# Optimization experiments

Measured on AMD Instinct MI355X. Metric: run time of the kernel, lower is better.

The kernel has to match this reference:

```python
import jax, jax.numpy as jnp
import numpy as np

IN_F = 256
OUT_F = 256
ALPHA = 0.2  # LeakyReLU negative slope


def _xavier(key, shape, gain=1.414):
    fan_in, fan_out = shape[0], shape[1]
    limit = gain * np.sqrt(6.0 / (fan_in + fan_out))
    return jax.random.uniform(key, shape, jnp.float32, -limit, limit)


def setup_inputs() -> dict:
    key = jax.random.key(0)
    k1, k2, k3, k4, k5, k6 = jax.random.split(key, 6)
    B, N = 8, 2048
    h = jax.random.normal(k1, (B, N, IN_F), jnp.float32)
    adj = jax.random.randint(k2, (B, N, N), 0, 2, jnp.int32)
    lrgt1 = jax.random.normal(k3, (B, N, OUT_F), jnp.float32)
    W1 = _xavier(k4, (IN_F, IN_F))
    W2 = _xavier(k5, (OUT_F, OUT_F))
    a = _xavier(k6, (2 * IN_F, 1))
    return {"h": h, "adj": adj, "lrgt1": lrgt1, "W1": W1, "W2": W2, "a": a}


def reference(h, adj, lrgt1, W1, W2, a):
    # Wh: [B,N,in], wlrgt: [B,N,out]
    Wh = jnp.matmul(h, W1)
    wlrgt = jnp.matmul(lrgt1, W2)
    # additive attention scores: e[b,i,j] = leaky_relu(Wh_i @ a1 + Wh_j @ a2)
    a1 = a[:IN_F, 0]   # [in]
    a2 = a[IN_F:, 0]   # [in]
    Wh1 = jnp.einsum('bnc,c->bn', Wh, a1)  # [B,N]
    Wh2 = jnp.einsum('bnc,c->bn', Wh, a2)  # [B,N]
    e = jax.nn.leaky_relu(Wh1[:, :, None] + Wh2[:, None, :], ALPHA)  # [B,N,N]
    neg = jnp.float32(-9e15)
    masked = jnp.where(adj > 0, e, neg)
    attention = jax.nn.softmax(masked, axis=2)
    # dropout p=0.0 / eval mode -> identity
    h_prime = jnp.matmul(attention, Wh)      # [B,N,in]
    gt_prime = jnp.matmul(attention, wlrgt)  # [B,N,out]
    return (jax.nn.elu(h_prime), jax.nn.elu(gt_prime))
```

## Files before the change

kernel.cpp:

```cpp
#include <hip/hip_runtime.h>
#include <hip/hip_bf16.h>

#define IN_F 256
#define NN   2048
#define BB   8

typedef unsigned short u16;
typedef __attribute__((ext_vector_type(8))) short short8x;
typedef __attribute__((ext_vector_type(4))) float float4x;

__device__ __forceinline__ u16 f2b(float f) {
    union { float f; unsigned int u; } x; x.f = f;
    unsigned int r = x.u + 0x7FFFu + ((x.u >> 16) & 1u);
    return (u16)(r >> 16);
}

__device__ __forceinline__ void transp_body(const float* __restrict__ src,
                                            u16* __restrict__ dst,
                                            int R, int C, int tid,
                                            float (*tile)[33])
{
    const int per = (R / 32) * (C / 32);
    const int b  = tid / per;
    const int tt = tid % per;
    const int jt = tt / (C / 32);
    const int ct = tt % (C / 32);
    src += (long)b * R * C;
    dst += (long)b * R * C;

    const int tx = threadIdx.x & 31, ty = threadIdx.x >> 5;
#pragma unroll
    for (int i = 0; i < 4; ++i)
        tile[ty + i * 8][tx] = src[(long)(jt * 32 + ty + i * 8) * C + ct * 32 + tx];
    __syncthreads();
#pragma unroll
    for (int i = 0; i < 4; ++i)
        dst[(long)(ct * 32 + ty + i * 8) * R + jt * 32 + tx] = f2b(tile[tx][ty + i * 8]);
}

__global__ __launch_bounds__(256) void prep(const float* __restrict__ h,
                                            const float* __restrict__ g,
                                            const float* __restrict__ W1,
                                            const float* __restrict__ W2,
                                            const float* __restrict__ a,
                                            u16* __restrict__ HbfT,
                                            u16* __restrict__ GbfT,
                                            u16* __restrict__ W1T,
                                            u16* __restrict__ W2T,
                                            float* __restrict__ v1,
                                            float* __restrict__ v2)
{
    __shared__ float tile[32][33];
    __shared__ float s1[IN_F], s2[IN_F];
    const int bid = blockIdx.x;

    if (bid < 4096) {
        transp_body(h, HbfT, NN, IN_F, bid, tile);
    } else if (bid < 8192) {
        transp_body(g, GbfT, NN, IN_F, bid - 4096, tile);
    } else if (bid < 8256) {
        transp_body(W1, W1T, IN_F, IN_F, bid - 8192, tile);
    } else if (bid < 8320) {
        transp_body(W2, W2T, IN_F, IN_F, bid - 8256, tile);
    } else {
        const int t = threadIdx.x;
        s1[t] = a[t];
        s2[t] = a[IN_F + t];
        __syncthreads();
        float acc1 = 0.f, acc2 = 0.f;
        for (int c = 0; c < IN_F; ++c) {
            float w = W1[t * IN_F + c];
            acc1 += w * s1[c];
            acc2 += w * s2[c];
        }
        v1[t] = acc1;
        v2[t] = acc2;
    }
}

__global__ __launch_bounds__(256) void rowdots(const float* __restrict__ h,
                                               const float* __restrict__ v1,
                                               const float* __restrict__ v2,
                                               float* __restrict__ Wh1,
                                               float* __restrict__ Wh2)
{
    const int wave = threadIdx.x >> 6;
    const int lane = threadIdx.x & 63;
    const long row = (long)blockIdx.x * 4 + wave;
    const int c0 = lane * 4;

    float4 v  = *(const float4*)(h + row * IN_F + c0);
    float4 a1 = *(const float4*)(v1 + c0);
    float4 a2 = *(const float4*)(v2 + c0);

    float s1 = v.x * a1.x + v.y * a1.y + v.z * a1.z + v.w * a1.w;
    float s2 = v.x * a2.x + v.y * a2.y + v.z * a2.z + v.w * a2.w;
#pragma unroll
    for (int off = 32; off; off >>= 1) {
        s1 += __shfl_xor(s1, off, 64);
        s2 += __shfl_xor(s2, off, 64);
    }
    if (lane == 0) { Wh1[row] = s1; Wh2[row] = s2; }
}

#define KSTEP(ksv, BC, BN_, AC, AN_, do_a, jnxt)                              \
    {                                                                         \
        if (do_a) {                                                           \
            _Pragma("unroll") for (int rt = 0; rt < 4; ++rt)                  \
                AN_[rt] = *(const short8x*)&ab[(((ksv) + 1) * 4 + rt) * 512 + lane * 8]; \
        }                                                                     \
        _Pragma("unroll") for (int ct = 0; ct < 4; ++ct)                      \
            BN_[ct] = *(const short8x*)(Bp + ct * 16 * NN + (jnxt));          \
        _Pragma("unroll") for (int rt = 0; rt < 4; ++rt)                      \
            _Pragma("unroll") for (int ct = 0; ct < 4; ++ct)                  \
                acc[rt][ct] = __builtin_amdgcn_mfma_f32_16x16x32_bf16(AC[rt], BC[ct], acc[rt][ct], 0, 0, 0); \
    }

#define CHUNKD2(KCH, ADJ, W4)                                                 \
    {                                                                         \
        const int j0 = (KCH) * 128;                                           \
        union { short8x v; u16 e[8]; } pk0, pk1;                              \
        _Pragma("unroll") for (int u = 0; u < 4; ++u) {                       \
            const float wf[4] = {W4[u].x, W4[u].y, W4[u].z, W4[u].w};         \
            const int   av[4] = {ADJ[u].x, ADJ[u].y, ADJ[u].z, ADJ[u].w};     \
            _Pragma("unroll") for (int c = 0; c < 4; ++c) {                   \
                float x = wh1rr + wf[c];                                      \
                float e = fmaxf(x, 0.2f * x);                                 \
                float p = __expf(e - mv);                                     \
                p = (av[c] > 0) ? p : 0.0f;                                   \
                lloc += p;                                                    \
                u16 fv = f2b(p);                                              \
                if (u < 2) pk0.e[u * 4 + c] = fv;                             \
                else       pk1.e[(u - 2) * 4 + c] = fv;                       \
            }                                                                 \
        }                                                                     \
        u16* ab = &Afrag[(KCH) & 1][0];                                       \
        *(short8x*)&ab[wbase0]       = pk0.v;                                 \
        *(short8x*)&ab[wbase0 + 128] = pk1.v;                                 \
        asm volatile("s_waitcnt lgkmcnt(0)\n\ts_barrier" ::: "memory");       \
        _Pragma("unroll") for (int rt = 0; rt < 4; ++rt)                      \
            A0[rt] = *(const short8x*)&ab[rt * 512 + lane * 8];               \
        KSTEP(0, B0, B1, A0, A1, 1, j0 + 1 * 32 + bq8)                        \
        KSTEP(1, B1, B0, A1, A0, 1, j0 + 2 * 32 + bq8)                        \
        KSTEP(2, B0, B1, A0, A1, 1, j0 + 3 * 32 + bq8)                        \
        KSTEP(3, B1, B0, A1, A0, 0, (((KCH) < 15) ? (j0 + 128) : j0) + bq8)   \
        if ((KCH) < 14) {                                                     \
            __builtin_amdgcn_sched_barrier(0);                                \
            const int jp = ((KCH) + 2) * 128 + sg * 16;                       \
            _Pragma("unroll") for (int u = 0; u < 4; ++u)                     \
                W4[u]  = *(const float4*)(wh2b + jp + u * 4);                 \
            _Pragma("unroll") for (int u = 0; u < 4; ++u)                     \
                ADJ[u] = *(const int4*)(adj + adjR + jp + u * 4);             \
        }                                                                     \
    }

__global__ __launch_bounds__(512, 2) void attn_mfma(
    const int* __restrict__ adj,
    const u16* __restrict__ HbfT, const u16* __restrict__ GbfT,
    const float* __restrict__ Wh1, const float* __restrict__ Wh2,
    u16* __restrict__ PH, u16* __restrict__ PG)
{
    const int t = threadIdx.x;
    const int wave = t >> 6, lane = t & 63;
    const int bswz = ((blockIdx.x & 7) << 5) | (blockIdx.x >> 3);
    const int b = bswz >> 5;
    const long gi0 = (long)bswz * 64;

    __shared__ __align__(16) u16 Afrag[2][8192];
    __shared__ float sred[512];
    __shared__ float ssc[65];

    const int rr = t >> 3, sg = t & 7;
    const long adjR = (gi0 + rr) * (long)NN;
    const float* wh2b = Wh2 + (long)b * NN;
    const float wh1rr = Wh1[gi0 + rr];

    {
        float4 w = *(const float4*)(wh2b + t * 4);
        sred[t] = fmaxf(fmaxf(w.x, w.y), fmaxf(w.z, w.w));
    }
    __syncthreads();
    if (t < 64) {
        float v = sred[t * 8];
#pragma unroll
        for (int k = 1; k < 8; ++k) v = fmaxf(v, sred[t * 8 + k]);
#pragma unroll
        for (int off = 32; off; off >>= 1) v = fmaxf(v, __shfl_xor(v, off, 64));
        if (t == 0) ssc[64] = v;
    }
    __syncthreads();
    const float mm = wh1rr + ssc[64];
    const float mv = (mm >= 0.f) ? mm : 0.2f * mm;

    const int wbase0 = ((sg >> 1) * 4 + (rr >> 4)) * 512
                     + ((rr & 15) + 16 * (2 * (sg & 1))) * 8;

    float4x acc[4][4];
#pragma unroll
    for (int rt = 0; rt < 4; ++rt)
#pragma unroll
        for (int ct = 0; ct < 4; ++ct) acc[rt][ct] = (float4x)0.0f;

    const int bn = lane & 15, bq = lane >> 4, bq8 = bq * 8;
    const long hbase = (long)b * IN_F * NN;
    const u16* Bp = ((wave < 4) ? HbfT : GbfT) + hbase
                  + (long)((wave & 3) * 64 + bn) * NN;

    float lloc = 0.f;

    short8x A0[4], A1[4], B0[4], B1[4];
    int4   adjA[4], adjB[4];
    float4 w4A[4], w4B[4];

#pragma unroll
    for (int u = 0; u < 4; ++u) {
        w4A[u]  = *(const float4*)(wh2b + sg * 16 + u * 4);
        adjA[u] = *(const int4*)(adj + adjR + sg * 16 + u * 4);
    }
#pragma unroll
    for (int u = 0; u < 4; ++u) {
        w4B[u]  = *(const float4*)(wh2b + 128 + sg * 16 + u * 4);
        adjB[u] = *(const int4*)(adj + adjR + 128 + sg * 16 + u * 4);
    }
#pragma unroll
    for (int ct = 0; ct < 4; ++ct)
        B0[ct] = *(const short8x*)(Bp + ct * 16 * NN + bq8);

    for (int kp = 0; kp < 8; ++kp) {
        CHUNKD2(kp * 2,     adjA, w4A)
        CHUNKD2(kp * 2 + 1, adjB, w4B)
    }

    sred[t] = lloc;
    __syncthreads();
    if (t < 64) {
        float v = sred[t * 8];
#pragma unroll
        for (int k = 1; k < 8; ++k) v += sred[t * 8 + k];
        ssc[t] = 1.0f / v;
    }
    __syncthreads();

    u16* dst = (wave < 4) ? PH : PG;
    const int colb = (wave & 3) * 64;
#pragma unroll
    for (int rt = 0; rt < 4; ++rt)
#pragma unroll
        for (int ct = 0; ct < 4; ++ct) {
            const int c = colb + ct * 16 + bn;
#pragma unroll
            for (int reg = 0; reg < 4; ++reg) {
                const int rl = rt * 16 + bq * 4 + reg;
                const float il = ssc[rl];
                const long row = gi0 + rl;
                dst[row * IN_F + c] = f2b(acc[rt][ct][reg] * il);
            }
        }
}

__global__ __launch_bounds__(256) void epi2(const u16* __restrict__ PH,
                                            const u16* __restrict__ PG,
                                            const u16* __restrict__ W1T,
                                            const u16* __restrict__ W2T,
                                            float* __restrict__ out)
{
    int bid = blockIdx.x;
    const u16* X;
    const u16* WT;
    float* o;
    if (bid < 512) { X = PH; WT = W1T; o = out; }
    else           { X = PG; WT = W2T; o = out + (long)BB * NN * IN_F; bid -= 512; }

    const int t = threadIdx.x;
    const int wave = t >> 6, lane = t & 63;
    const long i0 = (long)bid * 32;

    __shared__ __align__(16) u16 Afrag[8 * 2 * 64 * 8];

    const int m = t >> 3, ks0 = t & 7, rt0 = m >> 4, lm = m & 15;
    const u16* xp = X + (i0 + m) * IN_F + ks0 * 32;
#pragma unroll
    for (int q = 0; q < 4; ++q) {
        short8x v = *(const short8x*)(xp + q * 8);
        *(short8x*)&Afrag[((ks0 * 2 + rt0) * 64 + lm + q * 16) * 8] = v;
    }
    __syncthreads();

    float4x acc[2][4];
#pragma unroll
    for (int rt = 0; rt < 2; ++rt)
#pragma unroll
        for (int ct = 0; ct < 4; ++ct) acc[rt][ct] = (float4x)0.0f;

    const int bn = lane & 15, bq = lane >> 4;
#pragma unroll
    for (int ks = 0; ks < 8; ++ks) {
        short8x A0 = *(const short8x*)&Afrag[((ks * 2 + 0) * 64 + lane) * 8];
        short8x A1 = *(const short8x*)&Afrag[((ks * 2 + 1) * 64 + lane) * 8];
#pragma unroll
        for (int ct = 0; ct < 4; ++ct) {
            const int n = wave * 64 + ct * 16 + bn;
            short8x Bw = *(const short8x*)(WT + n * IN_F + ks * 32 + bq * 8);
            acc[0][ct] = __builtin_amdgcn_mfma_f32_16x16x32_bf16(A0, Bw, acc[0][ct], 0, 0, 0);
            acc[1][ct] = __builtin_amdgcn_mfma_f32_16x16x32_bf16(A1, Bw, acc[1][ct], 0, 0, 0);
        }
    }

#pragma unroll
    for (int rt = 0; rt < 2; ++rt)
#pragma unroll
        for (int ct = 0; ct < 4; ++ct) {
            const int n = wave * 64 + ct * 16 + bn;
#pragma unroll
            for (int reg = 0; reg < 4; ++reg) {
                const long row = i0 + rt * 16 + bq * 4 + reg;
                float v = acc[rt][ct][reg];
                v = (v > 0.f) ? v : (__expf(v) - 1.f);
                o[row * IN_F + n] = v;
            }
        }
}

extern "C" void kernel_launch(void* const* d_in, const int* in_sizes, int n_in,
                              void* d_out, int out_size, void* d_ws, size_t ws_size,
                              hipStream_t stream)
{
    int ih = -1, ig = -1, iadj = -1, iw1 = -1, iw2 = -1, ia = -1;
    for (int i = 0; i < n_in; ++i) {
        int s = in_sizes[i];
        if      (s == BB * NN * NN)   { if (iadj < 0) iadj = i; }
        else if (s == BB * NN * IN_F) { if (ih < 0) ih = i; else if (ig < 0) ig = i; }
        else if (s == IN_F * IN_F)    { if (iw1 < 0) iw1 = i; else if (iw2 < 0) iw2 = i; }
        else if (s == 2 * IN_F)       { if (ia < 0) ia = i; }
    }
    if (ih < 0 || ig < 0 || iadj < 0 || iw1 < 0 || iw2 < 0 || ia < 0) {
        ih = 0; iadj = 1; ig = 2; iw1 = 3; iw2 = 4; ia = 5;
    }
    const float* h     = (const float*)d_in[ih];
    const int*   adj   = (const int*)  d_in[iadj];
    const float* lrgt1 = (const float*)d_in[ig];
    const float* W1    = (const float*)d_in[iw1];
    const float* W2    = (const float*)d_in[iw2];
    const float* a     = (const float*)d_in[ia];
    float* out = (float*)d_out;

    float* ws   = (float*)d_ws;
    float* v1   = ws;
    float* v2   = v1 + IN_F;
    float* Wh1  = v2 + IN_F;
    float* Wh2  = Wh1 + BB * NN;
    u16* W1T  = (u16*)(Wh2 + BB * NN);
    u16* W2T  = W1T + IN_F * IN_F;
    u16* HbfT = W2T + IN_F * IN_F;
    u16* GbfT = HbfT + (long)BB * IN_F * NN;
    u16* PH   = GbfT + (long)BB * IN_F * NN;
    u16* PG   = PH + (long)BB * NN * IN_F;

    const int nrows = BB * NN;

    prep     <<<8321,        256, 0, stream>>>(h, lrgt1, W1, W2, a,
                                               HbfT, GbfT, W1T, W2T, v1, v2);
    rowdots  <<<nrows / 4,   256, 0, stream>>>(h, v1, v2, Wh1, Wh2);
    attn_mfma<<<nrows / 64,  512, 0, stream>>>(adj, HbfT, GbfT, Wh1, Wh2, PH, PG);
    epi2     <<<2 * nrows / 32, 256, 0, stream>>>(PH, PG, W1T, W2T, out);
}
```

Before: 313.6 us.

## Pack adjacency into bitmask, stage Wh2 in LDS, vectorize transpose

Adds a pre-pass kernel that ballots the int32 adjacency matrix into 64-bit masks stored in the output buffer as scratch. The attention kernel then reads one 32-bit mask word per chunk instead of 16 int4 loads, which removes register-held prefetch buffers and the heavy streaming of the int32 matrix inside the MFMA loop. Wh2 is staged once into shared memory rather than reloaded from global per chunk. The transpose in prep now uses float4 loads and ushort4 stores. The adjacency is still read once in full, but with simple coalesced nontemporal loads. Using d_out as scratch assumes the epilogue fully overwrites it afterwards.

New measurement: 344.3 us. 1.1x slower.

```diff
diff --git a/kernel.cpp b/kernel.cpp
--- a/kernel.cpp
+++ b/kernel.cpp
@@ -6,6 +6,7 @@
 #define BB   8
 
 typedef unsigned short u16;
+typedef unsigned long long u64;
 typedef __attribute__((ext_vector_type(8))) short short8x;
 typedef __attribute__((ext_vector_type(4))) float float4x;
 
@@ -15,10 +16,24 @@
     return (u16)(r >> 16);
 }
 
-__device__ __forceinline__ void transp_body(const float* __restrict__ src,
-                                            u16* __restrict__ dst,
-                                            int R, int C, int tid,
-                                            float (*tile)[33])
+__global__ __launch_bounds__(256) void adjpack(const int* __restrict__ adj,
+                                               u64* __restrict__ mask)
+{
+    const int wid  = (blockIdx.x * 256 + threadIdx.x) >> 6;
+    const int lane = threadIdx.x & 63;
+#pragma unroll 4
+    for (int it = 0; it < 64; ++it) {
+        const long s = (long)it * 8192 + wid;
+        const int v = __builtin_nontemporal_load(adj + s * 64 + lane);
+        const u64 m = __ballot(v > 0);
+        if (lane == 0) mask[s] = m;
+    }
+}
+
+__device__ __forceinline__ void transp_body4(const float* __restrict__ src,
+                                             u16* __restrict__ dst,
+                                             int R, int C, int tid,
+                                             float (*tile)[33])
 {
     const int per = (R / 32) * (C / 32);
     const int b  = tid / per;
@@ -28,14 +43,21 @@
     src += (long)b * R * C;
     dst += (long)b * R * C;
 
-    const int tx = threadIdx.x & 31, ty = threadIdx.x >> 5;
-#pragma unroll
-    for (int i = 0; i < 4; ++i)
-        tile[ty + i * 8][tx] = src[(long)(jt * 32 + ty + i * 8) * C + ct * 32 + tx];
-    __syncthreads();
-#pragma unroll
-    for (int i = 0; i < 4; ++i)
-        dst[(long)(ct * 32 + ty + i * 8) * R + jt * 32 + tx] = f2b(tile[tx][ty + i * 8]);
+    const int t = threadIdx.x;
+    const int lr = t >> 3, lc = (t & 7) * 4;
+    float4 v = *(const float4*)(src + (long)(jt * 32 + lr) * C + ct * 32 + lc);
+    tile[lr][lc + 0] = v.x;
+    tile[lr][lc + 1] = v.y;
+    tile[lr][lc + 2] = v.z;
+    tile[lr][lc + 3] = v.w;
+    __syncthreads();
+    const int c = t >> 3, r4 = (t & 7) * 4;
+    ushort4 o;
+    o.x = f2b(tile[r4 + 0][c]);
+    o.y = f2b(tile[r4 + 1][c]);
+    o.z = f2b(tile[r4 + 2][c]);
+    o.w = f2b(tile[r4 + 3][c]);
+    *(ushort4*)(dst + (long)(ct * 32 + c) * R + jt * 32 + r4) = o;
 }
 
 __global__ __launch_bounds__(256) void prep(const float* __restrict__ h,
@@ -55,13 +77,13 @@
     const int bid = blockIdx.x;
 
     if (bid < 4096) {
-        transp_body(h, HbfT, NN, IN_F, bid, tile);
+        transp_body4(h, HbfT, NN, IN_F, bid, tile);
     } else if (bid < 8192) {
-        transp_body(g, GbfT, NN, IN_F, bid - 4096, tile);
+        transp_body4(g, GbfT, NN, IN_F, bid - 4096, tile);
     } else if (bid < 8256) {
-        transp_body(W1, W1T, IN_F, IN_F, bid - 8192, tile);
+        transp_body4(W1, W1T, IN_F, IN_F, bid - 8192, tile);
     } else if (bid < 8320) {
-        transp_body(W2, W2T, IN_F, IN_F, bid - 8256, tile);
+        transp_body4(W2, W2T, IN_F, IN_F, bid - 8256, tile);
     } else {
         const int t = threadIdx.x;
         s1[t] = a[t];
@@ -116,24 +138,26 @@
                 acc[rt][ct] = __builtin_amdgcn_mfma_f32_16x16x32_bf16(AC[rt], BC[ct], acc[rt][ct], 0, 0, 0); \
     }
 
-#define CHUNKD2(KCH, ADJ, W4)                                                 \
+#define CHUNK9(KCH, MKC, MKN)                                                 \
     {                                                                         \
         const int j0 = (KCH) * 128;                                           \
+        const unsigned bits = (MKC) >> ((sg & 1) * 16);                       \
         union { short8x v; u16 e[8]; } pk0, pk1;                              \
         _Pragma("unroll") for (int u = 0; u < 4; ++u) {                       \
-            const float wf[4] = {W4[u].x, W4[u].y, W4[u].z, W4[u].w};         \
-            const int   av[4] = {ADJ[u].x, ADJ[u].y, ADJ[u].z, ADJ[u].w};     \
+            const float4 wv = *(const float4*)&wh2L[j0 + sg * 16 + u * 4];    \
+            const float wf[4] = {wv.x, wv.y, wv.z, wv.w};                     \
             _Pragma("unroll") for (int c = 0; c < 4; ++c) {                   \
                 float x = wh1rr + wf[c];                                      \
-                float e = fmaxf(x, 0.2f * x);                                 \
-                float p = __expf(e - mv);                                     \
-                p = (av[c] > 0) ? p : 0.0f;                                   \
+                float ev = fmaxf(x, 0.2f * x);                                \
+                float p = __expf(ev - mv);                                    \
+                p = ((bits >> (u * 4 + c)) & 1u) ? p : 0.0f;                  \
                 lloc += p;                                                    \
                 u16 fv = f2b(p);                                              \
                 if (u < 2) pk0.e[u * 4 + c] = fv;                             \
                 else       pk1.e[(u - 2) * 4 + c] = fv;                       \
             }                                                                 \
         }                                                                     \
+        if ((KCH) < 15) MKN = maskR[((KCH) + 1) * 4 + (sg >> 1)];             \
         u16* ab = &Afrag[(KCH) & 1][0];                                       \
         *(short8x*)&ab[wbase0]       = pk0.v;                                 \
         *(short8x*)&ab[wbase0 + 128] = pk1.v;                                 \
@@ -144,18 +168,10 @@
         KSTEP(1, B1, B0, A1, A0, 1, j0 + 2 * 32 + bq8)                        \
         KSTEP(2, B0, B1, A0, A1, 1, j0 + 3 * 32 + bq8)                        \
         KSTEP(3, B1, B0, A1, A0, 0, (((KCH) < 15) ? (j0 + 128) : j0) + bq8)   \
-        if ((KCH) < 14) {                                                     \
-            __builtin_amdgcn_sched_barrier(0);                                \
-            const int jp = ((KCH) + 2) * 128 + sg * 16;                       \
-            _Pragma("unroll") for (int u = 0; u < 4; ++u)                     \
-                W4[u]  = *(const float4*)(wh2b + jp + u * 4);                 \
-            _Pragma("unroll") for (int u = 0; u < 4; ++u)                     \
-                ADJ[u] = *(const int4*)(adj + adjR + jp + u * 4);             \
-        }                                                                     \
     }
 
 __global__ __launch_bounds__(512, 2) void attn_mfma(
-    const int* __restrict__ adj,
+    const unsigned* __restrict__ mask,
     const u16* __restrict__ HbfT, const u16* __restrict__ GbfT,
     const float* __restrict__ Wh1, const float* __restrict__ Wh2,
     u16* __restrict__ PH, u16* __restrict__ PG)
@@ -167,16 +183,18 @@
     const long gi0 = (long)bswz * 64;
 
     __shared__ __align__(16) u16 Afrag[2][8192];
+    __shared__ float wh2L[2048];
     __shared__ float sred[512];
     __shared__ float ssc[65];
 
     const int rr = t >> 3, sg = t & 7;
-    const long adjR = (gi0 + rr) * (long)NN;
     const float* wh2b = Wh2 + (long)b * NN;
     const float wh1rr = Wh1[gi0 + rr];
+    const unsigned* maskR = mask + (gi0 + rr) * 64;
 
     {
         float4 w = *(const float4*)(wh2b + t * 4);
+        *(float4*)&wh2L[t * 4] = w;
         sred[t] = fmaxf(fmaxf(w.x, w.y), fmaxf(w.z, w.w));
     }
     __syncthreads();
@@ -209,26 +227,17 @@
     float lloc = 0.f;
 
     short8x A0[4], A1[4], B0[4], B1[4];
-    int4   adjA[4], adjB[4];
-    float4 w4A[4], w4B[4];
-
-#pragma unroll
-    for (int u = 0; u < 4; ++u) {
-        w4A[u]  = *(const float4*)(wh2b + sg * 16 + u * 4);
-        adjA[u] = *(const int4*)(adj + adjR + sg * 16 + u * 4);
-    }
-#pragma unroll
-    for (int u = 0; u < 4; ++u) {
-        w4B[u]  = *(const float4*)(wh2b + 128 + sg * 16 + u * 4);
-        adjB[u] = *(const int4*)(adj + adjR + 128 + sg * 16 + u * 4);
-    }
+    unsigned mkA, mkB;
+
+    mkA = maskR[sg >> 1];
+    mkB = maskR[4 + (sg >> 1)];
 #pragma unroll
     for (int ct = 0; ct < 4; ++ct)
         B0[ct] = *(const short8x*)(Bp + ct * 16 * NN + bq8);
 
     for (int kp = 0; kp < 8; ++kp) {
-        CHUNKD2(kp * 2,     adjA, w4A)
-        CHUNKD2(kp * 2 + 1, adjB, w4B)
+        CHUNK9(kp * 2,     mkA, mkB)
+        CHUNK9(kp * 2 + 1, mkB, mkA)
     }
 
     sred[t] = lloc;
@@ -343,6 +352,9 @@
     const float* W2    = (const float*)d_in[iw2];
     const float* a     = (const float*)d_in[ia];
     float* out = (float*)d_out;
+
+    u64*      mask64 = (u64*)d_out;
+    unsigned* mask32 = (unsigned*)d_out;
 
     float* ws   = (float*)d_ws;
     float* v1   = ws;
@@ -358,9 +370,10 @@
 
     const int nrows = BB * NN;
 
+    adjpack  <<<2048,        256, 0, stream>>>(adj, mask64);
     prep     <<<8321,        256, 0, stream>>>(h, lrgt1, W1, W2, a,
                                                HbfT, GbfT, W1T, W2T, v1, v2);
     rowdots  <<<nrows / 4,   256, 0, stream>>>(h, v1, v2, Wh1, Wh2);
-    attn_mfma<<<nrows / 64,  512, 0, stream>>>(adj, HbfT, GbfT, Wh1, Wh2, PH, PG);
+    attn_mfma<<<nrows / 64,  512, 0, stream>>>(mask32, HbfT, GbfT, Wh1, Wh2, PH, PG);
     epi2     <<<2 * nrows / 32, 256, 0, stream>>>(PH, PG, W1T, W2T, out);
 }
```
